# Kernel optimization log

Measured on AMD Instinct MI355X. Metric: run time of the kernel, lower is better.

Reference implementation:

```python
import jax, jax.numpy as jnp
import numpy as np

N, D, H1, H2, C, K = 8192, 512, 1024, 512, 10, 64
EPS_BN = 1e-5  # torch BatchNorm1d default eps


def _bn(x, g, b):
    # BatchNorm1d in training mode: per-batch stats, biased variance
    mu = x.mean(axis=0)
    var = x.var(axis=0)
    return (x - mu) / jnp.sqrt(var + EPS_BN) * g + b


def _features(x, ibn_g, ibn_b, W1, b1, g1, bb1, W2, b2, g2, bb2):
    x = _bn(x, ibn_g, ibn_b)                    # input_norm
    h = _bn(jnp.tanh(x @ W1.T + b1), g1, bb1)   # layer 1: Linear -> Tanh -> BN
    h = _bn(jnp.tanh(h @ W2.T + b2), g2, bb2)   # layer 2
    return h                                    # [N, H2]


def _nona_self(fx, fn, y_ohe):
    # sim = -cdist(fx, fn); self-neighbor path (x == x_n): -inf diag + top-k mask
    sq_x = jnp.sum(fx * fx, axis=1)
    sq_n = jnp.sum(fn * fn, axis=1)
    d2 = jnp.maximum(sq_x[:, None] + sq_n[None, :] - 2.0 * (fx @ fn.T), 0.0)
    safe = d2 > 1e-9
    dist = jnp.where(safe, jnp.sqrt(jnp.where(safe, d2, 1.0)), 0.0)
    sim = -dist
    eye = jnp.eye(N, dtype=bool)
    sim = jnp.where(eye, -jnp.inf, sim)         # sim -= inf * I
    _, idx = jax.lax.top_k(sim, K)              # [N, K]
    keep = jnp.zeros((N, N), dtype=bool).at[jnp.arange(N)[:, None], idx].set(True)
    sim = jnp.where(keep, sim, -jnp.inf)        # KNNMask: non-topk -> -inf
    probs = jax.nn.softmax(sim, axis=1)
    return jnp.clip(probs @ y_ohe, 0.0, 1.0)


def setup_inputs() -> dict:
    key = jax.random.key(0)
    ks = jax.random.split(key, 6)
    x = jax.random.normal(ks[0], (N, D), dtype=jnp.float32)
    x_n = x + 0.0  # NONA self-neighbor mode requires x_n == x elementwise
    y_n = jax.random.randint(ks[1], (N,), 0, C, dtype=jnp.int32)
    s1 = 1.0 / np.sqrt(D)
    s2 = 1.0 / np.sqrt(H1)
    W1 = jax.random.uniform(ks[2], (H1, D), jnp.float32, -s1, s1)
    b1 = jax.random.uniform(ks[3], (H1,), jnp.float32, -s1, s1)
    W2 = jax.random.uniform(ks[4], (H2, H1), jnp.float32, -s2, s2)
    b2 = jax.random.uniform(ks[5], (H2,), jnp.float32, -s2, s2)
    return {
        "x": x, "x_n": x_n, "y_n": y_n,
        "ibn_g": jnp.ones((D,), jnp.float32), "ibn_b": jnp.zeros((D,), jnp.float32),
        "W1": W1, "b1": b1, "g1": jnp.ones((H1,), jnp.float32), "bb1": jnp.zeros((H1,), jnp.float32),
        "W2": W2, "b2": b2, "g2": jnp.ones((H2,), jnp.float32), "bb2": jnp.zeros((H2,), jnp.float32),
    }


def reference(x, x_n, y_n, ibn_g, ibn_b, W1, b1, g1, bb1, W2, b2, g2, bb2):
    fx = _features(x, ibn_g, ibn_b, W1, b1, g1, bb1, W2, b2, g2, bb2)
    fn = _features(x_n, ibn_g, ibn_b, W1, b1, g1, bb1, W2, b2, g2, bb2)
    y_ohe = jax.nn.one_hot(y_n, C, dtype=jnp.float32)
    return _nona_self(fx, fn, y_ohe)
```

## Files before the change

### kernel.cpp

```cpp
#include <hip/hip_runtime.h>
#include <math.h>

#define NROWS 8192
#define DIM   512
#define HID1  1024
#define HID2  512
#define NCLS  10
#define KTOP  64
#define KPACK 1024
#define KFULL 1536
#define EPSBAND 0.02f

typedef __attribute__((ext_vector_type(8))) short short8;
typedef __attribute__((ext_vector_type(4))) float f32x4;
typedef __attribute__((ext_vector_type(4))) double f64x4;

__device__ __forceinline__ unsigned short f2bf(float x) {
    unsigned u = __float_as_uint(x);
    u += 0x7FFFu + ((u >> 16) & 1u);
    return (unsigned short)(u >> 16);
}
__device__ __forceinline__ float bf2f(unsigned short h) {
    return __uint_as_float(((unsigned)h) << 16);
}

template <typename T>
__global__ __launch_bounds__(256) void col_stats_partial(
    const T* __restrict__ A, int F, int rowsPerBlock,
    double* __restrict__ pSum, double* __restrict__ pSqs)
{
    int c  = blockIdx.x * 256 + threadIdx.x;
    int r0 = blockIdx.y * rowsPerBlock;
    double s = 0.0, s2 = 0.0;
    for (int r = r0; r < r0 + rowsPerBlock; ++r) {
        double v = (double)A[(size_t)r * F + c];
        s  += v;
        s2 += v * v;
    }
    pSum[(size_t)blockIdx.y * F + c] = s;
    pSqs[(size_t)blockIdx.y * F + c] = s2;
}

__global__ __launch_bounds__(256) void col_stats_final(
    const double* __restrict__ pSum, const double* __restrict__ pSqs,
    const float* __restrict__ g, const float* __restrict__ b,
    double* __restrict__ scale, double* __restrict__ shift, int F, int nPart)
{
    int c = blockIdx.x * 256 + threadIdx.x;
    double s = 0.0, s2 = 0.0;
    for (int p = 0; p < nPart; ++p) {
        s  += pSum[(size_t)p * F + c];
        s2 += pSqs[(size_t)p * F + c];
    }
    double mean = s * (1.0 / NROWS);
    double var  = s2 * (1.0 / NROWS) - mean * mean;
    double sc   = (double)g[c] / sqrt(var + 1e-5);
    scale[c] = sc;
    shift[c] = (double)b[c] - mean * sc;
}

__global__ __launch_bounds__(256) void bn_apply_f32(
    const float* __restrict__ x, const double* __restrict__ scl, const double* __restrict__ sft,
    double* __restrict__ out)
{
    const int base = (blockIdx.x * 256 + threadIdx.x) * 4;
    float4 v = *(const float4*)&x[base];
    const int c = base & (DIM - 1);
    out[base + 0] = (double)v.x * scl[c + 0] + sft[c + 0];
    out[base + 1] = (double)v.y * scl[c + 1] + sft[c + 1];
    out[base + 2] = (double)v.z * scl[c + 2] + sft[c + 2];
    out[base + 3] = (double)v.w * scl[c + 3] + sft[c + 3];
}

__global__ __launch_bounds__(256) void bn_apply_f64(
    double* __restrict__ y, const double* __restrict__ scl, const double* __restrict__ sft,
    int mask)
{
    const int base = (blockIdx.x * 256 + threadIdx.x) * 4;
    const int c = base & mask;
    double2 v0 = *(const double2*)&y[base];
    double2 v1 = *(const double2*)&y[base + 2];
    v0.x = v0.x * scl[c + 0] + sft[c + 0];
    v0.y = v0.y * scl[c + 1] + sft[c + 1];
    v1.x = v1.x * scl[c + 2] + sft[c + 2];
    v1.y = v1.y * scl[c + 3] + sft[c + 3];
    *(double2*)&y[base]     = v0;
    *(double2*)&y[base + 2] = v1;
}

__global__ __launch_bounds__(256) void gemm_mfma_tanh(
    const double* __restrict__ A, const float* __restrict__ W, const float* __restrict__ bias,
    double* __restrict__ out, int Kd, int F)
{
    __shared__ double aS[32 * 132];
    __shared__ double bS[32 * 67];
    const int t = threadIdx.x;
    const int lane = t & 63;
    const int wv = t >> 6;
    const int nwg = gridDim.x;
    const int q = nwg >> 3;
    const int bid = blockIdx.x;
    const int wgid = (bid & 7) * q + (bid >> 3);
    const int fBlocks = F >> 6;
    const int mb = wgid / fBlocks;
    const int fb = wgid - mb * fBlocks;
    const int fBase = fb * 64;
    const int mBase = mb * 128;
    const int arow = t >> 1;
    const int akq  = (t & 1) * 16;
    const int wrow = t >> 2;
    const int wkq  = (t & 3) * 8;

    f64x4 acc[2][4];
    #pragma unroll
    for (int p = 0; p < 2; ++p)
        #pragma unroll
        for (int n = 0; n < 4; ++n) acc[p][n] = (f64x4){0.0, 0.0, 0.0, 0.0};

    double areg[16];
    float  wreg[8];

    auto stage_load = [&](int ch) {
        const int kb = ch << 5;
        const double* ap = &A[(size_t)(mBase + arow) * Kd + kb + akq];
        #pragma unroll
        for (int j = 0; j < 8; ++j) {
            double2 v = *(const double2*)(ap + 2 * j);
            areg[2 * j] = v.x; areg[2 * j + 1] = v.y;
        }
        const float4* wp = (const float4*)&W[(size_t)(fBase + wrow) * Kd + kb + wkq];
        float4 w0 = wp[0], w1 = wp[1];
        wreg[0] = w0.x; wreg[1] = w0.y; wreg[2] = w0.z; wreg[3] = w0.w;
        wreg[4] = w1.x; wreg[5] = w1.y; wreg[6] = w1.z; wreg[7] = w1.w;
    };
    auto stage_write = [&]() {
        #pragma unroll
        for (int i = 0; i < 16; ++i)
            aS[(akq + i) * 132 + arow] = areg[i];
        #pragma unroll
        for (int i = 0; i < 8; ++i)
            bS[(wkq + i) * 67 + wrow] = (double)wreg[i];
    };
    auto compute = [&]() {
        #pragma unroll
        for (int k4 = 0; k4 < 8; ++k4) {
            const int kk = k4 * 4 + (lane >> 4);
            double a0 = aS[kk * 132 + wv * 16 + (lane & 15)];
            double a1 = aS[kk * 132 + 64 + wv * 16 + (lane & 15)];
            #pragma unroll
            for (int n = 0; n < 4; ++n) {
                double b = bS[kk * 67 + n * 16 + (lane & 15)];
                acc[0][n] = __builtin_amdgcn_mfma_f64_16x16x4f64(a0, b, acc[0][n], 0, 0, 0);
                acc[1][n] = __builtin_amdgcn_mfma_f64_16x16x4f64(a1, b, acc[1][n], 0, 0, 0);
            }
        }
    };

    const int nChunks = Kd >> 5;
    stage_load(0);
    stage_write();
    __syncthreads();
    for (int ch = 0; ch < nChunks; ++ch) {
        const bool hn = (ch + 1 < nChunks);
        if (hn) stage_load(ch + 1);
        compute();
        __syncthreads();
        if (hn) {
            stage_write();
            __syncthreads();
        }
    }

    #pragma unroll
    for (int p = 0; p < 2; ++p) {
        #pragma unroll
        for (int n = 0; n < 4; ++n) {
            const int f = fBase + n * 16 + (lane & 15);
            const double bz = (double)bias[f];
            #pragma unroll
            for (int r = 0; r < 4; ++r) {
                const int m = mBase + p * 64 + wv * 16 + (lane >> 4) * 4 + r;
                out[(size_t)m * F + f] = tanh(acc[p][n][r] + bz);
            }
        }
    }
}

__global__ __launch_bounds__(256) void pack_features(
    const double* __restrict__ y2, const double* __restrict__ scl, const double* __restrict__ sft,
    unsigned short* __restrict__ R, float* __restrict__ sqf)
{
    __shared__ double red[4];
    const int r = blockIdx.x;
    const int t = threadIdx.x;
    const int wid = t >> 6, lane = t & 63;
    const int c = t * 2;
    double2 y  = *(const double2*)&y2[(size_t)r * HID2 + c];
    double2 s2 = *(const double2*)&scl[c];
    double2 h2 = *(const double2*)&sft[c];
    double f0 = y.x * s2.x + h2.x;
    double f1 = y.y * s2.y + h2.y;
    unsigned short hi0 = f2bf((float)f0);
    unsigned short hi1 = f2bf((float)f1);
    unsigned short lo0 = f2bf((float)(f0 - (double)bf2f(hi0)));
    unsigned short lo1 = f2bf((float)(f1 - (double)bf2f(hi1)));
    unsigned short* Rr = R + (size_t)r * KPACK;
    Rr[c]           = hi0; Rr[c + 1]           = hi1;
    Rr[HID2 + c]    = lo0; Rr[HID2 + c + 1]    = lo1;
    double s = f0 * f0 + f1 * f1;
    #pragma unroll
    for (int off = 32; off > 0; off >>= 1) s += __shfl_down(s, off);
    if (lane == 0) red[wid] = s;
    __syncthreads();
    if (t == 0) sqf[r] = (float)(red[0] + red[1] + red[2] + red[3]);
}

__global__ __launch_bounds__(256, 1) void sim_mfma(
    const unsigned short* __restrict__ R, const float* __restrict__ sqf,
    float* __restrict__ simbuf, int rowBase)
{
    __shared__ unsigned short aT[2][128 * 64];
    __shared__ unsigned short bT[2][256 * 64];
    const int t = threadIdx.x;
    const int wid = t >> 6, lane = t & 63;
    const int wr = wid >> 1, wc = wid & 1;
    const int bid  = blockIdx.x;
    const int wgid = (bid & 7) * 32 + (bid >> 3);
    const int ib = wgid & 7;
    const int jb = wgid >> 3;
    const int iBase = rowBase + ib * 128;
    const int jBase = jb * 256;
    const int srow = lane >> 3;
    const int skk  = (((lane & 7) ^ srow) * 8);

    f32x4 acc[4][8];
    #pragma unroll
    for (int m = 0; m < 4; ++m)
        #pragma unroll
        for (int n = 0; n < 8; ++n) acc[m][n] = (f32x4){0.f, 0.f, 0.f, 0.f};

    auto STAGE = [&](int buf, int kt) {
        const int k0 = kt * 64;
        const int aSrc = (k0 < 512)  ? k0 : (k0 - 512);
        const int bSrc = (k0 < 1024) ? k0 : (k0 - 1024);
        #pragma unroll
        for (int c = 0; c < 4; ++c) {
            const int g = wid * 4 + c;
            const unsigned short* gp = R + (size_t)(iBase + g * 8 + srow) * KPACK + aSrc + skk;
            __builtin_amdgcn_global_load_lds((const __attribute__((address_space(1))) void*)gp,
                (__attribute__((address_space(3))) void*)&aT[buf][g * 512], 16, 0, 0);
        }
        #pragma unroll
        for (int c = 0; c < 8; ++c) {
            const int g = wid * 8 + c;
            const unsigned short* gp = R + (size_t)(jBase + g * 8 + srow) * KPACK + bSrc + skk;
            __builtin_amdgcn_global_load_lds((const __attribute__((address_space(1))) void*)gp,
                (__attribute__((address_space(3))) void*)&bT[buf][g * 512], 16, 0, 0);
        }
    };

    STAGE(0, 0);
    __syncthreads();
    int cur = 0;
    const int nKT = KFULL / 64;
    for (int kt = 0; kt < nKT; ++kt) {
        if (kt + 1 < nKT) STAGE(cur ^ 1, kt + 1);
        #pragma unroll
        for (int ks = 0; ks < 2; ++ks) {
            const int ck = ((ks * 4 + (lane >> 4)) ^ (lane & 7)) * 8;
            short8 aF[4], bF[8];
            #pragma unroll
            for (int m = 0; m < 4; ++m) {
                int rA = wr * 64 + m * 16 + (lane & 15);
                aF[m] = *(const short8*)&aT[cur][rA * 64 + ck];
            }
            #pragma unroll
            for (int n = 0; n < 8; ++n) {
                int rB = wc * 128 + n * 16 + (lane & 15);
                bF[n] = *(const short8*)&bT[cur][rB * 64 + ck];
            }
            #pragma unroll
            for (int m = 0; m < 4; ++m)
                #pragma unroll
                for (int n = 0; n < 8; ++n)
                    acc[m][n] = __builtin_amdgcn_mfma_f32_16x16x32_bf16(aF[m], bF[n], acc[m][n], 0, 0, 0);
        }
        __syncthreads();
        cur ^= 1;
    }

    #pragma unroll
    for (int m = 0; m < 4; ++m) {
        #pragma unroll
        for (int n = 0; n < 8; ++n) {
            int j = jBase + wc * 128 + n * 16 + (lane & 15);
            float sqj = sqf[j];
            #pragma unroll
            for (int r = 0; r < 4; ++r) {
                int i = iBase + wr * 64 + m * 16 + (lane >> 4) * 4 + r;
                float d2 = sqf[i] + sqj - 2.0f * acc[m][n][r];
                d2 = fmaxf(d2, 0.f);
                float s = (i == j) ? -INFINITY : -d2;
                simbuf[(size_t)(i - rowBase) * NROWS + j] = s;
            }
        }
    }
}

__device__ __forceinline__ unsigned fKey(float v) {
    unsigned b = __float_as_uint(v);
    return (b & 0x80000000u) ? ~b : (b | 0x80000000u);
}
__device__ __forceinline__ float keyToFloat(unsigned k) {
    unsigned b = (k & 0x80000000u) ? (k ^ 0x80000000u) : ~k;
    return __uint_as_float(b);
}

__global__ __launch_bounds__(256) void topk_refine(
    const float* __restrict__ simbuf,
    const double* __restrict__ y2, const double* __restrict__ scl, const double* __restrict__ sft,
    const int* __restrict__ labels, float* __restrict__ out, int rowBase)
{
    __shared__ unsigned redU[4], redL[4];
    __shared__ int      totArr[36];
    __shared__ float    redF[4];
    __shared__ float    cls[NCLS];
    __shared__ int      bandJ[128];
    __shared__ double   bandD2[128];
    __shared__ unsigned char keepB[128];
    __shared__ int      bandCnt;

    const int t = threadIdx.x;
    const int wid = t >> 6, lane = t & 63;
    const int row = blockIdx.x;
    const int gi = rowBase + row;
    const float* srow = simbuf + (size_t)row * NROWS;

    unsigned key[32];
    #pragma unroll
    for (int ii = 0; ii < 8; ++ii) {
        float4 v = ((const float4*)srow)[t + ii * 256];
        key[ii * 4 + 0] = fKey(v.x);
        key[ii * 4 + 1] = fKey(v.y);
        key[ii * 4 + 2] = fKey(v.z);
        key[ii * 4 + 3] = fKey(v.w);
    }
    const unsigned infKey = fKey(-INFINITY);

    unsigned kmax = 0u, kmin = 0xFFFFFFFFu;
    #pragma unroll
    for (int ii = 0; ii < 32; ++ii) {
        kmax = max(kmax, key[ii]);
        kmin = min(kmin, (key[ii] == infKey) ? 0xFFFFFFFFu : key[ii]);
    }
    #pragma unroll
    for (int off = 32; off > 0; off >>= 1) {
        kmax = max(kmax, (unsigned)__shfl_down(kmax, off));
        kmin = min(kmin, (unsigned)__shfl_down(kmin, off));
    }
    if (lane == 0) { redU[wid] = kmax; redL[wid] = kmin; }
    if (t == 0) bandCnt = 0;
    if (t < NCLS) cls[t] = 0.f;
    if (t < 36) totArr[t] = 0;
    __syncthreads();
    kmax = max(max(redU[0], redU[1]), max(redU[2], redU[3]));
    kmin = min(min(redL[0], redL[1]), min(redL[2], redL[3]));
    float d2min = fmaxf(-keyToFloat(kmax), 0.f);
    float distMin = (d2min > 1e-9f) ? sqrtf(d2min) : 0.f;

    unsigned lo = kmin, hi = kmax;
    int it = 0;
    while (lo < hi) {
        unsigned mid = lo + ((hi - lo + 1u) >> 1);
        int cnt = 0;
        #pragma unroll
        for (int ii = 0; ii < 32; ++ii) cnt += (key[ii] >= mid) ? 1 : 0;
        #pragma unroll
        for (int off = 32; off > 0; off >>= 1) cnt += __shfl_down(cnt, off);
        if (lane == 0) atomicAdd(&totArr[it], cnt);
        __syncthreads();
        int tot = totArr[it];
        if (tot >= KTOP) lo = mid; else hi = mid - 1u;
        ++it;
    }
    const float s64 = keyToFloat(lo);
    const unsigned Ku = fKey(s64 + EPSBAND);
    const unsigned Kl = fKey(s64 - EPSBAND);

    {
        int cnt = 0;
        #pragma unroll
        for (int ii = 0; ii < 32; ++ii) cnt += (key[ii] >= Ku) ? 1 : 0;
        #pragma unroll
        for (int off = 32; off > 0; off >>= 1) cnt += __shfl_down(cnt, off);
        if (lane == 0) atomicAdd(&totArr[34], cnt);
    }
    #pragma unroll
    for (int ii = 0; ii < 8; ++ii) {
        #pragma unroll
        for (int q2 = 0; q2 < 4; ++q2) {
            unsigned k = key[ii * 4 + q2];
            if (k >= Kl && k < Ku) {
                int pos = atomicAdd(&bandCnt, 1);
                if (pos < 128) bandJ[pos] = (t + ii * 256) * 4 + q2;
            }
        }
    }
    __syncthreads();
    const int nSafe = totArr[34];
    const int Rslots = KTOP - nSafe;
    const int nb = min(bandCnt, 128);

    for (int c2 = wid; c2 < nb; c2 += 4) {
        int j = bandJ[c2];
        double s = 0.0;
        for (int d = lane; d < HID2; d += 64) {
            double sc = scl[d], sh = sft[d];
            double fi = y2[(size_t)gi * HID2 + d] * sc + sh;
            double fj = y2[(size_t)j  * HID2 + d] * sc + sh;
            double df = fi - fj;
            s += df * df;
        }
        #pragma unroll
        for (int off = 32; off > 0; off >>= 1) s += __shfl_down(s, off);
        if (lane == 0) bandD2[c2] = s;
    }
    __syncthreads();

    for (int c2 = t; c2 < nb; c2 += 256) {
        double d2c = bandD2[c2];
        int jc = bandJ[c2];
        int rank = 0;
        for (int q2 = 0; q2 < nb; ++q2) {
            double dq = bandD2[q2];
            rank += (dq < d2c || (dq == d2c && bandJ[q2] < jc)) ? 1 : 0;
        }
        keepB[c2] = (rank < Rslots) ? 1 : 0;
    }
    __syncthreads();

    float S = 0.f;
    #pragma unroll
    for (int ii = 0; ii < 8; ++ii) {
        #pragma unroll
        for (int q2 = 0; q2 < 4; ++q2) {
            unsigned k = key[ii * 4 + q2];
            if (k >= Ku) {
                float d2 = -keyToFloat(k);
                float dist = (d2 > 1e-9f) ? sqrtf(d2) : 0.f;
                float w = expf(distMin - dist);
                S += w;
                atomicAdd(&cls[labels[(t + ii * 256) * 4 + q2]], w);
            }
        }
    }
    for (int c2 = t; c2 < nb; c2 += 256) {
        if (keepB[c2]) {
            double dd = bandD2[c2];
            float dist = (dd > 1e-9) ? (float)sqrt(dd) : 0.f;
            float w = expf(distMin - dist);
            S += w;
            atomicAdd(&cls[labels[bandJ[c2]]], w);
        }
    }
    #pragma unroll
    for (int off = 32; off > 0; off >>= 1) S += __shfl_down(S, off);
    if (lane == 0) redF[wid] = S;
    __syncthreads();
    float Stot = redF[0] + redF[1] + redF[2] + redF[3];

    if (t < NCLS) {
        float p = cls[t] / Stot;
        out[(size_t)gi * NCLS + t] = fminf(fmaxf(p, 0.f), 1.f);
    }
}

extern "C" void kernel_launch(void* const* d_in, const int* in_sizes, int n_in,
                              void* d_out, int out_size, void* d_ws, size_t ws_size,
                              hipStream_t stream)
{
    const float* x     = (const float*)d_in[0];
    const int*   y_n   = (const int*)d_in[2];
    const float* ibn_g = (const float*)d_in[3];
    const float* ibn_b = (const float*)d_in[4];
    const float* W1    = (const float*)d_in[5];
    const float* b1    = (const float*)d_in[6];
    const float* g1    = (const float*)d_in[7];
    const float* bb1   = (const float*)d_in[8];
    const float* W2    = (const float*)d_in[9];
    const float* b2    = (const float*)d_in[10];
    const float* g2    = (const float*)d_in[11];
    const float* bb2   = (const float*)d_in[12];
    float* out = (float*)d_out;

    char* ws = (char*)d_ws;
    double*         y1   = (double*)(ws);
    float*          simb = (float*)(ws);
    unsigned short* Rp   = (unsigned short*)(ws + 33554432);
    double*         y2   = (double*)(ws + 67108864);
    double*         xbn  = y2;
    double*         pSum = (double*)(ws + 100663296);
    double*         pSqs = (double*)(ws + 101187584);
    double*         prm  = (double*)(ws + 101711872);
    double* scale0 = prm;           double* shift0 = prm + 1024;
    double* scale1 = prm + 2048;    double* shift1 = prm + 3072;
    double* scale2 = prm + 4096;    double* shift2 = prm + 5120;
    float*          sqf  = (float*)(ws + 101761024);

    dim3 blk(256);
    const int RPB = NROWS / 64;

    col_stats_partial<float><<<dim3(DIM / 256, 64), blk, 0, stream>>>(x, DIM, RPB, pSum, pSqs);
    col_stats_final<<<dim3(DIM / 256), blk, 0, stream>>>(pSum, pSqs, ibn_g, ibn_b, scale0, shift0, DIM, 64);
    bn_apply_f32<<<dim3(NROWS * DIM / 1024), blk, 0, stream>>>(x, scale0, shift0, xbn);
    gemm_mfma_tanh<<<dim3((NROWS / 128) * (HID1 / 64)), blk, 0, stream>>>(xbn, W1, b1, y1, DIM, HID1);
    col_stats_partial<double><<<dim3(HID1 / 256, 64), blk, 0, stream>>>(y1, HID1, RPB, pSum, pSqs);
    col_stats_final<<<dim3(HID1 / 256), blk, 0, stream>>>(pSum, pSqs, g1, bb1, scale1, shift1, HID1, 64);
    bn_apply_f64<<<dim3(NROWS * HID1 / 1024), blk, 0, stream>>>(y1, scale1, shift1, HID1 - 1);
    gemm_mfma_tanh<<<dim3((NROWS / 128) * (HID2 / 64)), blk, 0, stream>>>(y1, W2, b2, y2, HID1, HID2);
    col_stats_partial<double><<<dim3(HID2 / 256, 64), blk, 0, stream>>>(y2, HID2, RPB, pSum, pSqs);
    col_stats_final<<<dim3(HID2 / 256), blk, 0, stream>>>(pSum, pSqs, g2, bb2, scale2, shift2, HID2, 64);
    pack_features<<<dim3(NROWS), blk, 0, stream>>>(y2, scale2, shift2, Rp, sqf);
    for (int ch = 0; ch < 8; ++ch) {
        int rowBase = ch * 1024;
        sim_mfma<<<dim3(256), blk, 0, stream>>>(Rp, sqf, simb, rowBase);
        topk_refine<<<dim3(1024), blk, 0, stream>>>(simb, y2, scale2, shift2, y_n, out, rowBase);
    }
}
```

Before: 1.302 ms.

## Double-buffer fp64 feature GEMM and overlap async LDS loads in distance GEMM

The fp64 tanh GEMM now uses two LDS buffers with a K-chunk of 16, so it needs one barrier per iteration instead of two. It also stores W as float in shared memory to cut LDS footprint. The bf16 distance GEMM swaps the full __syncthreads after each tile for a partial vmcnt wait that lets the next tile's global_load_lds prefetch stay in flight, and raises wave priority around the MFMA block. This risks correctness if the vmcnt(12) count does not match the per-thread load count.

```diff
diff --git a/kernel.cpp b/kernel.cpp
--- a/kernel.cpp
+++ b/kernel.cpp
@@ -92,8 +92,8 @@
     const double* __restrict__ A, const float* __restrict__ W, const float* __restrict__ bias,
     double* __restrict__ out, int Kd, int F)
 {
-    __shared__ double aS[32 * 132];
-    __shared__ double bS[32 * 67];
+    __shared__ double aS[2][16 * 132];
+    __shared__ float  bS[2][16 * 68];
     const int t = threadIdx.x;
     const int lane = t & 63;
     const int wv = t >> 6;
@@ -107,9 +107,9 @@
     const int fBase = fb * 64;
     const int mBase = mb * 128;
     const int arow = t >> 1;
-    const int akq  = (t & 1) * 16;
+    const int akq  = (t & 1) * 8;
     const int wrow = t >> 2;
-    const int wkq  = (t & 3) * 8;
+    const int wkq  = (t & 3) * 4;
 
     f64x4 acc[2][4];
     #pragma unroll
@@ -117,58 +117,55 @@
         #pragma unroll
         for (int n = 0; n < 4; ++n) acc[p][n] = (f64x4){0.0, 0.0, 0.0, 0.0};
 
-    double areg[16];
-    float  wreg[8];
+    double areg[8];
+    float  wreg[4];
 
     auto stage_load = [&](int ch) {
-        const int kb = ch << 5;
+        const int kb = ch << 4;
         const double* ap = &A[(size_t)(mBase + arow) * Kd + kb + akq];
         #pragma unroll
-        for (int j = 0; j < 8; ++j) {
+        for (int j = 0; j < 4; ++j) {
             double2 v = *(const double2*)(ap + 2 * j);
             areg[2 * j] = v.x; areg[2 * j + 1] = v.y;
         }
-        const float4* wp = (const float4*)&W[(size_t)(fBase + wrow) * Kd + kb + wkq];
-        float4 w0 = wp[0], w1 = wp[1];
+        float4 w0 = *(const float4*)&W[(size_t)(fBase + wrow) * Kd + kb + wkq];
         wreg[0] = w0.x; wreg[1] = w0.y; wreg[2] = w0.z; wreg[3] = w0.w;
-        wreg[4] = w1.x; wreg[5] = w1.y; wreg[6] = w1.z; wreg[7] = w1.w;
     };
-    auto stage_write = [&]() {
-        #pragma unroll
-        for (int i = 0; i < 16; ++i)
-            aS[(akq + i) * 132 + arow] = areg[i];
+    auto stage_write = [&](int buf) {
         #pragma unroll
         for (int i = 0; i < 8; ++i)
-            bS[(wkq + i) * 67 + wrow] = (double)wreg[i];
+            aS[buf][(akq + i) * 132 + arow] = areg[i];
+        #pragma unroll
+        for (int i = 0; i < 4; ++i)
+            bS[buf][(wkq + i) * 68 + wrow] = wreg[i];
     };
-    auto compute = [&]() {
-        #pragma unroll
-        for (int k4 = 0; k4 < 8; ++k4) {
+    auto compute = [&](int buf) {
+        #pragma unroll
+        for (int k4 = 0; k4 < 4; ++k4) {
             const int kk = k4 * 4 + (lane >> 4);
-            double a0 = aS[kk * 132 + wv * 16 + (lane & 15)];
-            double a1 = aS[kk * 132 + 64 + wv * 16 + (lane & 15)];
+            double a0 = aS[buf][kk * 132 + wv * 16 + (lane & 15)];
+            double a1 = aS[buf][kk * 132 + 64 + wv * 16 + (lane & 15)];
             #pragma unroll
             for (int n = 0; n < 4; ++n) {
-                double b = bS[kk * 67 + n * 16 + (lane & 15)];
+                double b = (double)bS[buf][kk * 68 + n * 16 + (lane & 15)];
                 acc[0][n] = __builtin_amdgcn_mfma_f64_16x16x4f64(a0, b, acc[0][n], 0, 0, 0);
                 acc[1][n] = __builtin_amdgcn_mfma_f64_16x16x4f64(a1, b, acc[1][n], 0, 0, 0);
             }
         }
     };
 
-    const int nChunks = Kd >> 5;
+    const int nChunks = Kd >> 4;
     stage_load(0);
-    stage_write();
-    __syncthreads();
+    stage_write(0);
+    __syncthreads();
+    int cur = 0;
     for (int ch = 0; ch < nChunks; ++ch) {
         const bool hn = (ch + 1 < nChunks);
         if (hn) stage_load(ch + 1);
-        compute();
+        compute(cur);
+        if (hn) stage_write(cur ^ 1);
         __syncthreads();
-        if (hn) {
-            stage_write();
-            __syncthreads();
-        }
+        cur ^= 1;
     }
 
     #pragma unroll
@@ -258,13 +255,7 @@
                 (__attribute__((address_space(3))) void*)&bT[buf][g * 512], 16, 0, 0);
         }
     };
-
-    STAGE(0, 0);
-    __syncthreads();
-    int cur = 0;
-    const int nKT = KFULL / 64;
-    for (int kt = 0; kt < nKT; ++kt) {
-        if (kt + 1 < nKT) STAGE(cur ^ 1, kt + 1);
+    auto MFMA_TILE = [&](int buf) {
         #pragma unroll
         for (int ks = 0; ks < 2; ++ks) {
             const int ck = ((ks * 4 + (lane >> 4)) ^ (lane & 7)) * 8;
@@ -272,22 +263,42 @@
             #pragma unroll
             for (int m = 0; m < 4; ++m) {
                 int rA = wr * 64 + m * 16 + (lane & 15);
-                aF[m] = *(const short8*)&aT[cur][rA * 64 + ck];
+                aF[m] = *(const short8*)&aT[buf][rA * 64 + ck];
             }
             #pragma unroll
             for (int n = 0; n < 8; ++n) {
                 int rB = wc * 128 + n * 16 + (lane & 15);
-                bF[n] = *(const short8*)&bT[cur][rB * 64 + ck];
-            }
+                bF[n] = *(const short8*)&bT[buf][rB * 64 + ck];
+            }
+            __builtin_amdgcn_s_setprio(1);
             #pragma unroll
             for (int m = 0; m < 4; ++m)
                 #pragma unroll
                 for (int n = 0; n < 8; ++n)
                     acc[m][n] = __builtin_amdgcn_mfma_f32_16x16x32_bf16(aF[m], bF[n], acc[m][n], 0, 0, 0);
-        }
-        __syncthreads();
+            __builtin_amdgcn_s_setprio(0);
+        }
+    };
+
+    const int nKT = KFULL / 64;
+    STAGE(0, 0);
+    int cur = 0;
+    for (int kt = 0; kt < nKT - 1; ++kt) {
+        STAGE(cur ^ 1, kt + 1);
+        asm volatile("s_waitcnt vmcnt(12)" ::: "memory");
+        __builtin_amdgcn_s_barrier();
+        asm volatile("" ::: "memory");
+        __builtin_amdgcn_sched_barrier(0);
+        MFMA_TILE(cur);
+        asm volatile("" ::: "memory");
+        __builtin_amdgcn_s_barrier();
         cur ^= 1;
     }
+    asm volatile("s_waitcnt vmcnt(0)" ::: "memory");
+    __builtin_amdgcn_s_barrier();
+    asm volatile("" ::: "memory");
+    __builtin_amdgcn_sched_barrier(0);
+    MFMA_TILE(cur);
 
     #pragma unroll
     for (int m = 0; m < 4; ++m) {
```

New measurement: 1.362 ms. 4.7% more time.
